# Performance work log

Hardware: AMD Instinct MI355X
Metric: run time of the kernel (lower is better)

Reference implementation:

```python
import jax, jax.numpy as jnp
import numpy as np

N, D, K = 500000, 128, 16
TEMPERATURE = 0.5
NUM_ITER = 10
EPS = 1e-8


def _row_normalize(x, eps=0.0):
    return x / (jnp.linalg.norm(x, axis=1, keepdims=True) + eps)


def _compute(data, mu, num_iter):
    # data: [N, D] (already L2-normalized rows), mu: [K, D]
    for _ in range(num_iter):
        mu = _row_normalize(mu)                      # mu / ||mu||
        # pairwise cosine similarity: re-normalizes both operands
        dn = _row_normalize(data)
        mn = _row_normalize(mu)
        cos = dn @ mn.T                              # [N, K]
        r = jax.nn.softmax(-TEMPERATURE * cos, axis=1)  # [N, K]
        cluster_r = r.sum(axis=0)                    # [K]
        cluster_mean = r.T @ data                    # [K, D]
        mu = cluster_mean / cluster_r[:, None]       # diag(1/cluster_r) @ mean
    return mu, r


def setup_inputs() -> dict:
    key = jax.random.key(0)
    k1, k2 = jax.random.split(key)
    embeddings = jax.random.normal(k1, (N, D), dtype=jnp.float32)
    mu_init = jax.random.uniform(k2, (K, D), dtype=jnp.float32)
    return {"embeddings": embeddings, "mu_init": mu_init}


def reference(embeddings, mu_init):
    data = embeddings / (jnp.linalg.norm(embeddings, axis=1) + EPS)[:, None]
    mu_init, _ = _compute(data, mu_init, 1)   # one warm-up iteration
    mu, r = _compute(data, mu_init, NUM_ITER)
    return (mu, r)
```

## Files before the change

kernel.cpp:

```cpp
#include <hip/hip_runtime.h>
#include <math.h>


#define N_ROWS 500000
#define D 128
#define K 16
#define TEMP 0.5f
#define EPSV 1e-8f
#define TILE 64
#define BLK 256
#define RL 20
#define NITER 11
#define NTILES ((N_ROWS + TILE - 1) / TILE)
#define NB 512

typedef const __attribute__((address_space(1))) float4* gas_f4;
typedef __attribute__((address_space(3))) float4* las_f4;

__device__ __forceinline__ void gl_lds16(const float4* g, float4* l) {
    __builtin_amdgcn_global_load_lds((gas_f4)g, (las_f4)l, 16, 0, 0);
}

__global__ void k_init(const float* __restrict__ mu0,
                       float* __restrict__ mn,
                       float* __restrict__ accum) {
    __shared__ float m1[K * D];
    __shared__ float inv[K];
    const int t = threadIdx.x;
    for (int i = t; i < K * D + K; i += 256) accum[i] = 0.0f;
    if (t < K) {
        float ss = 0.0f;
        for (int d = 0; d < D; ++d) { float v = mu0[t * D + d]; ss += v * v; }
        inv[t] = 1.0f / sqrtf(ss);
    }
    __syncthreads();
    for (int i = t; i < K * D; i += 256) m1[i] = mu0[i] * inv[i / D];
    __syncthreads();
    if (t < K) {
        float ss = 0.0f;
        for (int d = 0; d < D; ++d) { float v = m1[t * D + d]; ss += v * v; }
        inv[t] = 1.0f / sqrtf(ss);
    }
    __syncthreads();
    for (int i = t; i < K * D; i += 256) mn[i] = m1[i] * inv[i / D];
}

__global__ __launch_bounds__(BLK) void k_main(const float* __restrict__ e,
                                              const float* __restrict__ mn,
                                              float* __restrict__ accum,
                                              float* __restrict__ r_out,
                                              int write_r) {
    __shared__ float4 elds[2][TILE * 32];
    __shared__ float  mn_lds[K * D];
    __shared__ float  rlds[TILE * RL];

    const int t  = threadIdx.x;
    const int wv = t >> 6;
    const int ln = t & 63;
    const int g  = t >> 2;
    const int q  = t & 3;
    const int d4 = t & 31;
    const int kg = t >> 5;

    const float4* __restrict__ e4 = (const float4*)e;

    int tile = blockIdx.x;
    {
        #pragma unroll
        for (int i = 0; i < 8; ++i) {
            const int sigma = wv * 512 + i * 64 + ln;
            const int sg = sigma >> 5, s = sigma & 31;
            int row = tile * TILE + sg; if (row > N_ROWS - 1) row = N_ROWS - 1;
            gl_lds16(e4 + row * 32 + (s ^ (sg & 31)), &elds[0][wv * 512 + i * 64]);
        }
        const float4* mg = (const float4*)mn;
        float4* ml = (float4*)mn_lds;
        ml[t] = mg[t]; ml[t + 256] = mg[t + 256];
    }
    asm volatile("s_waitcnt lgkmcnt(0)" ::: "memory");
    __builtin_amdgcn_sched_barrier(0);
    __builtin_amdgcn_s_barrier();
    __builtin_amdgcn_sched_barrier(0);

    const float4* __restrict__ ml4 = (const float4*)mn_lds;

    float acc[2][4] = {{0.f,0.f,0.f,0.f},{0.f,0.f,0.f,0.f}};
    float crq[4] = {0.f, 0.f, 0.f, 0.f};

    int buf = 0;
    for (; tile < NTILES; tile += NB, buf ^= 1) {
        const int base = tile * TILE;
        const int nt = tile + NB;
        const bool hasnext = nt < NTILES;
        if (hasnext) {
            #pragma unroll
            for (int i = 0; i < 8; ++i) {
                const int sigma = wv * 512 + i * 64 + ln;
                const int sg = sigma >> 5, s = sigma & 31;
                int row = nt * TILE + sg; if (row > N_ROWS - 1) row = N_ROWS - 1;
                gl_lds16(e4 + row * 32 + (s ^ (sg & 31)), &elds[buf ^ 1][wv * 512 + i * 64]);
            }
            asm volatile("s_waitcnt vmcnt(8)" ::: "memory");
        } else {
            asm volatile("s_waitcnt vmcnt(0)" ::: "memory");
        }
        __builtin_amdgcn_sched_barrier(0);
        __builtin_amdgcn_s_barrier();
        __builtin_amdgcn_sched_barrier(0);

        const float4* __restrict__ eb = (const float4*)elds[buf];
        const int row = base + g;
        const bool valid = row < N_ROWS;

        float dot[K];
        #pragma unroll
        for (int k = 0; k < K; ++k) dot[k] = 0.0f;
        float ss = 0.0f;
        #pragma unroll
        for (int c = 0; c < 8; ++c) {
            const float4 ev = eb[(g << 5) + ((c * 4 + q) ^ (g & 31))];
            ss += ev.x * ev.x + ev.y * ev.y + ev.z * ev.z + ev.w * ev.w;
            #pragma unroll
            for (int k = 0; k < K; ++k) {
                const float4 m = ml4[k * 32 + c * 4 + q];
                dot[k] += ev.x * m.x + ev.y * m.y + ev.z * m.z + ev.w * m.w;
            }
        }
        #pragma unroll
        for (int k = 0; k < K; ++k) {
            dot[k] += __shfl_xor(dot[k], 1);
            dot[k] += __shfl_xor(dot[k], 2);
        }
        ss += __shfl_xor(ss, 1);
        ss += __shfl_xor(ss, 2);

        const float nrm  = sqrtf(ss);
        const float binv = 1.0f / nrm;
        const float ainv = 1.0f / (nrm + EPSV);

        float mx = -1e30f;
        #pragma unroll
        for (int k = 0; k < K; ++k) {
            dot[k] = -TEMP * dot[k] * binv;
            mx = fmaxf(mx, dot[k]);
        }
        float sum = 0.0f;
        #pragma unroll
        for (int k = 0; k < K; ++k) { dot[k] = __expf(dot[k] - mx); sum += dot[k]; }
        const float isum = 1.0f / sum;

        float rsel[4] = {0.f, 0.f, 0.f, 0.f};
        #pragma unroll
        for (int qq = 0; qq < 4; ++qq) {
            if (q == qq) {
                #pragma unroll
                for (int j = 0; j < 4; ++j) rsel[j] = dot[qq * 4 + j];
            }
        }
        float4 rv;
        rv.x = valid ? rsel[0] * isum : 0.0f;
        rv.y = valid ? rsel[1] * isum : 0.0f;
        rv.z = valid ? rsel[2] * isum : 0.0f;
        rv.w = valid ? rsel[3] * isum : 0.0f;
        crq[0] += rv.x; crq[1] += rv.y; crq[2] += rv.z; crq[3] += rv.w;

        float4 rt;
        rt.x = rv.x * ainv; rt.y = rv.y * ainv;
        rt.z = rv.z * ainv; rt.w = rv.w * ainv;
        *(float4*)&rlds[g * RL + q * 4] = rt;

        if (write_r && valid)
            ((float4*)(r_out + row * K))[q] = rv;

        asm volatile("s_waitcnt lgkmcnt(0)" ::: "memory");
        __builtin_amdgcn_sched_barrier(0);
        __builtin_amdgcn_s_barrier();
        __builtin_amdgcn_sched_barrier(0);

        #pragma unroll 8
        for (int p = 0; p < TILE; ++p) {
            const float4 ev = eb[(p << 5) + (d4 ^ (p & 31))];
            const float2 rr = *(const float2*)&rlds[p * RL + 2 * kg];
            acc[0][0] += rr.x * ev.x; acc[0][1] += rr.x * ev.y;
            acc[0][2] += rr.x * ev.z; acc[0][3] += rr.x * ev.w;
            acc[1][0] += rr.y * ev.x; acc[1][1] += rr.y * ev.y;
            acc[1][2] += rr.y * ev.z; acc[1][3] += rr.y * ev.w;
        }
        __builtin_amdgcn_sched_barrier(0);
        __builtin_amdgcn_s_barrier();
        __builtin_amdgcn_sched_barrier(0);
    }

    #pragma unroll
    for (int kk = 0; kk < 2; ++kk)
        #pragma unroll
        for (int j = 0; j < 4; ++j)
            atomicAdd(&accum[(2 * kg + kk) * D + d4 * 4 + j], acc[kk][j]);

    __syncthreads();
    *(float4*)&rlds[t * 4] = *(float4*)crq;
    __syncthreads();
    if (t < K) {
        const int qq = t >> 2, jj = t & 3;
        float s = 0.0f;
        #pragma unroll 4
        for (int i = 0; i < 64; ++i) s += rlds[(i * 4 + qq) * 4 + jj];
        atomicAdd(&accum[K * D + t], s);
    }
}

__global__ void k_update(float* __restrict__ accum,
                         float* __restrict__ mn,
                         float* __restrict__ mu_out,
                         int last) {
    __shared__ float mu[K * D];
    __shared__ float inv[K];
    const int t = threadIdx.x;
    for (int i = t; i < K * D; i += 256)
        mu[i] = accum[i] / accum[K * D + i / D];
    __syncthreads();
    if (last) {
        for (int i = t; i < K * D; i += 256) mu_out[i] = mu[i];
    } else {
        if (t < K) {
            float ssq = 0.0f;
            for (int d = 0; d < D; ++d) { float v = mu[t * D + d]; ssq += v * v; }
            inv[t] = 1.0f / sqrtf(ssq);
        }
        __syncthreads();
        for (int i = t; i < K * D; i += 256) mu[i] *= inv[i / D];
        __syncthreads();
        if (t < K) {
            float ssq = 0.0f;
            for (int d = 0; d < D; ++d) { float v = mu[t * D + d]; ssq += v * v; }
            inv[t] = 1.0f / sqrtf(ssq);
        }
        __syncthreads();
        for (int i = t; i < K * D; i += 256) mn[i] = mu[i] * inv[i / D];
    }
    __syncthreads();
    for (int i = t; i < K * D + K; i += 256) accum[i] = 0.0f;
}

extern "C" void kernel_launch(void* const* d_in, const int* in_sizes, int n_in,
                              void* d_out, int out_size, void* d_ws, size_t ws_size,
                              hipStream_t stream) {
    const float* e   = (const float*)d_in[0];
    const float* mu0 = (const float*)d_in[1];
    float* out = (float*)d_out;
    float* ws  = (float*)d_ws;

    float* mn    = ws;
    float* accum = ws + K * D;
    float* r_out = out + K * D;

    hipLaunchKernelGGL(k_init, dim3(1), dim3(256), 0, stream, mu0, mn, accum);
    for (int it = 0; it < NITER; ++it) {
        const int last = (it == NITER - 1) ? 1 : 0;
        hipLaunchKernelGGL(k_main, dim3(NB), dim3(BLK), 0, stream,
                           e, mn, accum, r_out, last);
        hipLaunchKernelGGL(k_update, dim3(1), dim3(256), 0, stream,
                           accum, mn, out, last);
    }
}
```

Before: 2.087 ms.

## Split dot products across waves by D-slice and read centroids from scalar memory

```diff
diff --git a/kernel.cpp b/kernel.cpp
--- a/kernel.cpp
+++ b/kernel.cpp
@@ -9,7 +9,6 @@
 #define EPSV 1e-8f
 #define TILE 64
 #define BLK 256
-#define RL 20
 #define NITER 11
 #define NTILES ((N_ROWS + TILE - 1) / TILE)
 #define NB 512
@@ -51,54 +50,46 @@
                                               float* __restrict__ r_out,
                                               int write_r) {
     __shared__ float4 elds[2][TILE * 32];
-    __shared__ float  mn_lds[K * D];
-    __shared__ float  rlds[TILE * RL];
-
-    const int t  = threadIdx.x;
-    const int wv = t >> 6;
-    const int ln = t & 63;
-    const int g  = t >> 2;
-    const int q  = t & 3;
-    const int d4 = t & 31;
-    const int kg = t >> 5;
-
-    const float4* __restrict__ e4 = (const float4*)e;
+    __shared__ float4 plds[4 * TILE * 4];
+
+    const int t   = threadIdx.x;
+    const int wvu = __builtin_amdgcn_readfirstlane(t >> 6);
+    const int ln  = t & 63;
+    const int g   = t >> 2;
+    const int q   = t & 3;
+    const int ph  = (t >> 5) & 1;
+    const int d4b = t & 31;
+
+    const float4* __restrict__ e4  = (const float4*)e;
+    const float4* __restrict__ mn4 = (const float4*)mn;
 
     int tile = blockIdx.x;
-    {
-        #pragma unroll
-        for (int i = 0; i < 8; ++i) {
-            const int sigma = wv * 512 + i * 64 + ln;
-            const int sg = sigma >> 5, s = sigma & 31;
-            int row = tile * TILE + sg; if (row > N_ROWS - 1) row = N_ROWS - 1;
-            gl_lds16(e4 + row * 32 + (s ^ (sg & 31)), &elds[0][wv * 512 + i * 64]);
-        }
-        const float4* mg = (const float4*)mn;
-        float4* ml = (float4*)mn_lds;
-        ml[t] = mg[t]; ml[t + 256] = mg[t + 256];
-    }
-    asm volatile("s_waitcnt lgkmcnt(0)" ::: "memory");
-    __builtin_amdgcn_sched_barrier(0);
-    __builtin_amdgcn_s_barrier();
-    __builtin_amdgcn_sched_barrier(0);
-
-    const float4* __restrict__ ml4 = (const float4*)mn_lds;
-
-    float acc[2][4] = {{0.f,0.f,0.f,0.f},{0.f,0.f,0.f,0.f}};
+    #pragma unroll
+    for (int i = 0; i < 8; ++i) {
+        const int sigma = wvu * 512 + i * 64 + ln;
+        const int sg = sigma >> 5, s = sigma & 31;
+        int row = tile * TILE + sg; if (row > N_ROWS - 1) row = N_ROWS - 1;
+        gl_lds16(e4 + row * 32 + (s ^ (sg & 31)), &elds[0][wvu * 512 + i * 64]);
+    }
+
+    float acc[4][4];
+    #pragma unroll
+    for (int a = 0; a < 4; ++a)
+        #pragma unroll
+        for (int b = 0; b < 4; ++b) acc[a][b] = 0.0f;
     float crq[4] = {0.f, 0.f, 0.f, 0.f};
 
     int buf = 0;
     for (; tile < NTILES; tile += NB, buf ^= 1) {
         const int base = tile * TILE;
         const int nt = tile + NB;
-        const bool hasnext = nt < NTILES;
-        if (hasnext) {
+        if (nt < NTILES) {
             #pragma unroll
             for (int i = 0; i < 8; ++i) {
-                const int sigma = wv * 512 + i * 64 + ln;
+                const int sigma = wvu * 512 + i * 64 + ln;
                 const int sg = sigma >> 5, s = sigma & 31;
                 int row = nt * TILE + sg; if (row > N_ROWS - 1) row = N_ROWS - 1;
-                gl_lds16(e4 + row * 32 + (s ^ (sg & 31)), &elds[buf ^ 1][wv * 512 + i * 64]);
+                gl_lds16(e4 + row * 32 + (s ^ (sg & 31)), &elds[buf ^ 1][wvu * 512 + i * 64]);
             }
             asm volatile("s_waitcnt vmcnt(8)" ::: "memory");
         } else {
@@ -109,82 +100,96 @@
         __builtin_amdgcn_sched_barrier(0);
 
         const float4* __restrict__ eb = (const float4*)elds[buf];
+
+        float dp[K];
+        #pragma unroll
+        for (int k = 0; k < K; ++k) dp[k] = 0.0f;
+        #pragma unroll
+        for (int c = 0; c < 8; ++c) {
+            const float4 ev = eb[(ln << 5) + (((c << 2) + wvu) ^ (ln & 31))];
+            #pragma unroll
+            for (int k = 0; k < K; ++k) {
+                const float4 m = mn4[k * 32 + (c << 2) + wvu];
+                dp[k] += ev.x * m.x + ev.y * m.y + ev.z * m.z + ev.w * m.w;
+            }
+        }
+        #pragma unroll
+        for (int j = 0; j < 4; ++j) {
+            float4 v;
+            v.x = dp[j * 4 + 0]; v.y = dp[j * 4 + 1];
+            v.z = dp[j * 4 + 2]; v.w = dp[j * 4 + 3];
+            plds[wvu * 256 + ln * 4 + ((j + (ln >> 1)) & 3)] = v;
+        }
+        asm volatile("s_waitcnt lgkmcnt(0)" ::: "memory");
+        __builtin_amdgcn_sched_barrier(0);
+        __builtin_amdgcn_s_barrier();
+        __builtin_amdgcn_sched_barrier(0);
+
         const int row = base + g;
         const bool valid = row < N_ROWS;
-
-        float dot[K];
-        #pragma unroll
-        for (int k = 0; k < K; ++k) dot[k] = 0.0f;
-        float ss = 0.0f;
+        float4 dsum = {0.f, 0.f, 0.f, 0.f};
+        #pragma unroll
+        for (int w2 = 0; w2 < 4; ++w2) {
+            const float4 v = plds[w2 * 256 + g * 4 + ((q + (g >> 1)) & 3)];
+            dsum.x += v.x; dsum.y += v.y; dsum.z += v.z; dsum.w += v.w;
+        }
+        float ssp = 0.0f;
         #pragma unroll
         for (int c = 0; c < 8; ++c) {
-            const float4 ev = eb[(g << 5) + ((c * 4 + q) ^ (g & 31))];
-            ss += ev.x * ev.x + ev.y * ev.y + ev.z * ev.z + ev.w * ev.w;
-            #pragma unroll
-            for (int k = 0; k < K; ++k) {
-                const float4 m = ml4[k * 32 + c * 4 + q];
-                dot[k] += ev.x * m.x + ev.y * m.y + ev.z * m.z + ev.w * m.w;
-            }
-        }
-        #pragma unroll
-        for (int k = 0; k < K; ++k) {
-            dot[k] += __shfl_xor(dot[k], 1);
-            dot[k] += __shfl_xor(dot[k], 2);
-        }
-        ss += __shfl_xor(ss, 1);
-        ss += __shfl_xor(ss, 2);
-
-        const float nrm  = sqrtf(ss);
+            const float4 evv = eb[(g << 5) + (((q << 3) + c) ^ (g & 31))];
+            ssp += evv.x * evv.x + evv.y * evv.y + evv.z * evv.z + evv.w * evv.w;
+        }
+        ssp += __shfl_xor(ssp, 1);
+        ssp += __shfl_xor(ssp, 2);
+        const float nrm  = sqrtf(ssp);
         const float binv = 1.0f / nrm;
         const float ainv = 1.0f / (nrm + EPSV);
 
-        float mx = -1e30f;
-        #pragma unroll
-        for (int k = 0; k < K; ++k) {
-            dot[k] = -TEMP * dot[k] * binv;
-            mx = fmaxf(mx, dot[k]);
-        }
-        float sum = 0.0f;
-        #pragma unroll
-        for (int k = 0; k < K; ++k) { dot[k] = __expf(dot[k] - mx); sum += dot[k]; }
-        const float isum = 1.0f / sum;
-
-        float rsel[4] = {0.f, 0.f, 0.f, 0.f};
-        #pragma unroll
-        for (int qq = 0; qq < 4; ++qq) {
-            if (q == qq) {
-                #pragma unroll
-                for (int j = 0; j < 4; ++j) rsel[j] = dot[qq * 4 + j];
-            }
-        }
-        float4 rv;
-        rv.x = valid ? rsel[0] * isum : 0.0f;
-        rv.y = valid ? rsel[1] * isum : 0.0f;
-        rv.z = valid ? rsel[2] * isum : 0.0f;
-        rv.w = valid ? rsel[3] * isum : 0.0f;
-        crq[0] += rv.x; crq[1] += rv.y; crq[2] += rv.z; crq[3] += rv.w;
+        float d0 = -TEMP * binv * dsum.x;
+        float d1 = -TEMP * binv * dsum.y;
+        float d2 = -TEMP * binv * dsum.z;
+        float d3 = -TEMP * binv * dsum.w;
+        float mx = fmaxf(fmaxf(d0, d1), fmaxf(d2, d3));
+        mx = fmaxf(mx, __shfl_xor(mx, 1));
+        mx = fmaxf(mx, __shfl_xor(mx, 2));
+        float e0 = __expf(d0 - mx), e1 = __expf(d1 - mx);
+        float e2 = __expf(d2 - mx), e3 = __expf(d3 - mx);
+        float sm = e0 + e1 + e2 + e3;
+        sm += __shfl_xor(sm, 1);
+        sm += __shfl_xor(sm, 2);
+        const float isum = 1.0f / sm;
+        const float r0 = valid ? e0 * isum : 0.0f;
+        const float r1 = valid ? e1 * isum : 0.0f;
+        const float r2 = valid ? e2 * isum : 0.0f;
+        const float r3 = valid ? e3 * isum : 0.0f;
+        crq[0] += r0; crq[1] += r1; crq[2] += r2; crq[3] += r3;
 
         float4 rt;
-        rt.x = rv.x * ainv; rt.y = rv.y * ainv;
-        rt.z = rv.z * ainv; rt.w = rv.w * ainv;
-        *(float4*)&rlds[g * RL + q * 4] = rt;
-
-        if (write_r && valid)
+        rt.x = r0 * ainv; rt.y = r1 * ainv; rt.z = r2 * ainv; rt.w = r3 * ainv;
+        plds[g * 4 + ((q + (g >> 1)) & 3)] = rt;
+
+        if (write_r && valid) {
+            float4 rv; rv.x = r0; rv.y = r1; rv.z = r2; rv.w = r3;
             ((float4*)(r_out + row * K))[q] = rv;
-
+        }
         asm volatile("s_waitcnt lgkmcnt(0)" ::: "memory");
         __builtin_amdgcn_sched_barrier(0);
         __builtin_amdgcn_s_barrier();
         __builtin_amdgcn_sched_barrier(0);
 
         #pragma unroll 8
-        for (int p = 0; p < TILE; ++p) {
-            const float4 ev = eb[(p << 5) + (d4 ^ (p & 31))];
-            const float2 rr = *(const float2*)&rlds[p * RL + 2 * kg];
+        for (int i = 0; i < 32; ++i) {
+            const int p = ph * 32 + i;
+            const float4 ev = eb[(p << 5) + (d4b ^ i)];
+            const float4 rr = plds[p * 4 + ((wvu + (p >> 1)) & 3)];
             acc[0][0] += rr.x * ev.x; acc[0][1] += rr.x * ev.y;
             acc[0][2] += rr.x * ev.z; acc[0][3] += rr.x * ev.w;
             acc[1][0] += rr.y * ev.x; acc[1][1] += rr.y * ev.y;
             acc[1][2] += rr.y * ev.z; acc[1][3] += rr.y * ev.w;
+            acc[2][0] += rr.z * ev.x; acc[2][1] += rr.z * ev.y;
+            acc[2][2] += rr.z * ev.z; acc[2][3] += rr.z * ev.w;
+            acc[3][0] += rr.w * ev.x; acc[3][1] += rr.w * ev.y;
+            acc[3][2] += rr.w * ev.z; acc[3][3] += rr.w * ev.w;
         }
         __builtin_amdgcn_sched_barrier(0);
         __builtin_amdgcn_s_barrier();
@@ -192,19 +197,21 @@
     }
 
     #pragma unroll
-    for (int kk = 0; kk < 2; ++kk)
+    for (int kk = 0; kk < 4; ++kk)
         #pragma unroll
         for (int j = 0; j < 4; ++j)
-            atomicAdd(&accum[(2 * kg + kk) * D + d4 * 4 + j], acc[kk][j]);
-
-    __syncthreads();
-    *(float4*)&rlds[t * 4] = *(float4*)crq;
+            atomicAdd(&accum[(wvu * 4 + kk) * D + d4b * 4 + j], acc[kk][j]);
+
+    __syncthreads();
+    float* fld = (float*)plds;
+    fld[t * 4 + 0] = crq[0]; fld[t * 4 + 1] = crq[1];
+    fld[t * 4 + 2] = crq[2]; fld[t * 4 + 3] = crq[3];
     __syncthreads();
     if (t < K) {
         const int qq = t >> 2, jj = t & 3;
         float s = 0.0f;
         #pragma unroll 4
-        for (int i = 0; i < 64; ++i) s += rlds[(i * 4 + qq) * 4 + jj];
+        for (int i = 0; i < 64; ++i) s += fld[(i * 4 + qq) * 4 + jj];
         atomicAdd(&accum[K * D + t], s);
     }
 }
```

Result: slower. 2.546 ms (+22.0%).

## Double block size to 512 threads and split work across 8 lanes per row

Applied to the files above, without the earlier changes.

```diff
diff --git a/kernel.cpp b/kernel.cpp
--- a/kernel.cpp
+++ b/kernel.cpp
@@ -8,8 +8,8 @@
 #define TEMP 0.5f
 #define EPSV 1e-8f
 #define TILE 64
-#define BLK 256
-#define RL 20
+#define BLK 512
+#define RL 18
 #define NITER 11
 #define NTILES ((N_ROWS + TILE - 1) / TILE)
 #define NB 512
@@ -51,56 +51,51 @@
                                               float* __restrict__ r_out,
                                               int write_r) {
     __shared__ float4 elds[2][TILE * 32];
-    __shared__ float  mn_lds[K * D];
+    __shared__ float4 mn_lds4[K * 32];
     __shared__ float  rlds[TILE * RL];
 
     const int t  = threadIdx.x;
     const int wv = t >> 6;
     const int ln = t & 63;
-    const int g  = t >> 2;
-    const int q  = t & 3;
+    const int g  = t >> 3;
+    const int o  = t & 7;
     const int d4 = t & 31;
-    const int kg = t >> 5;
+    const int kp = (t >> 5) & 7;
+    const int ph = t >> 8;
 
     const float4* __restrict__ e4 = (const float4*)e;
 
     int tile = blockIdx.x;
-    {
-        #pragma unroll
-        for (int i = 0; i < 8; ++i) {
-            const int sigma = wv * 512 + i * 64 + ln;
-            const int sg = sigma >> 5, s = sigma & 31;
-            int row = tile * TILE + sg; if (row > N_ROWS - 1) row = N_ROWS - 1;
-            gl_lds16(e4 + row * 32 + (s ^ (sg & 31)), &elds[0][wv * 512 + i * 64]);
-        }
-        const float4* mg = (const float4*)mn;
-        float4* ml = (float4*)mn_lds;
-        ml[t] = mg[t]; ml[t + 256] = mg[t + 256];
-    }
+    #pragma unroll
+    for (int i = 0; i < 4; ++i) {
+        const int sigma = wv * 256 + i * 64 + ln;
+        const int sg = sigma >> 5, s = sigma & 31;
+        int row = tile * TILE + sg; if (row > N_ROWS - 1) row = N_ROWS - 1;
+        gl_lds16(e4 + row * 32 + (s ^ (sg & 31)), &elds[0][sigma]);
+    }
+    mn_lds4[t] = ((const float4*)mn)[t & 511];
     asm volatile("s_waitcnt lgkmcnt(0)" ::: "memory");
     __builtin_amdgcn_sched_barrier(0);
     __builtin_amdgcn_s_barrier();
     __builtin_amdgcn_sched_barrier(0);
 
-    const float4* __restrict__ ml4 = (const float4*)mn_lds;
-
-    float acc[2][4] = {{0.f,0.f,0.f,0.f},{0.f,0.f,0.f,0.f}};
-    float crq[4] = {0.f, 0.f, 0.f, 0.f};
+    float acc0[4] = {0.f,0.f,0.f,0.f};
+    float acc1[4] = {0.f,0.f,0.f,0.f};
+    float cr0 = 0.f, cr1 = 0.f;
 
     int buf = 0;
     for (; tile < NTILES; tile += NB, buf ^= 1) {
         const int base = tile * TILE;
         const int nt = tile + NB;
-        const bool hasnext = nt < NTILES;
-        if (hasnext) {
+        if (nt < NTILES) {
             #pragma unroll
-            for (int i = 0; i < 8; ++i) {
-                const int sigma = wv * 512 + i * 64 + ln;
+            for (int i = 0; i < 4; ++i) {
+                const int sigma = wv * 256 + i * 64 + ln;
                 const int sg = sigma >> 5, s = sigma & 31;
                 int row = nt * TILE + sg; if (row > N_ROWS - 1) row = N_ROWS - 1;
-                gl_lds16(e4 + row * 32 + (s ^ (sg & 31)), &elds[buf ^ 1][wv * 512 + i * 64]);
+                gl_lds16(e4 + row * 32 + (s ^ (sg & 31)), &elds[buf ^ 1][sigma]);
             }
-            asm volatile("s_waitcnt vmcnt(8)" ::: "memory");
+            asm volatile("s_waitcnt vmcnt(4)" ::: "memory");
         } else {
             asm volatile("s_waitcnt vmcnt(0)" ::: "memory");
         }
@@ -112,65 +107,70 @@
         const int row = base + g;
         const bool valid = row < N_ROWS;
 
-        float dot[K];
-        #pragma unroll
-        for (int k = 0; k < K; ++k) dot[k] = 0.0f;
+        float dp[16];
+        #pragma unroll
+        for (int k = 0; k < 16; ++k) dp[k] = 0.0f;
         float ss = 0.0f;
         #pragma unroll
-        for (int c = 0; c < 8; ++c) {
-            const float4 ev = eb[(g << 5) + ((c * 4 + q) ^ (g & 31))];
+        for (int c = 0; c < 4; ++c) {
+            const float4 ev = eb[(g << 5) + (((c << 3) + o) ^ (g & 31))];
             ss += ev.x * ev.x + ev.y * ev.y + ev.z * ev.z + ev.w * ev.w;
             #pragma unroll
-            for (int k = 0; k < K; ++k) {
-                const float4 m = ml4[k * 32 + c * 4 + q];
-                dot[k] += ev.x * m.x + ev.y * m.y + ev.z * m.z + ev.w * m.w;
+            for (int k = 0; k < 16; ++k) {
+                const float4 m = mn_lds4[k * 32 + (c << 3) + o];
+                dp[k] += ev.x * m.x + ev.y * m.y + ev.z * m.z + ev.w * m.w;
             }
         }
         #pragma unroll
-        for (int k = 0; k < K; ++k) {
-            dot[k] += __shfl_xor(dot[k], 1);
-            dot[k] += __shfl_xor(dot[k], 2);
+        for (int k = 0; k < 16; ++k) {
+            dp[k] += __shfl_xor(dp[k], 1);
+            dp[k] += __shfl_xor(dp[k], 2);
         }
         ss += __shfl_xor(ss, 1);
         ss += __shfl_xor(ss, 2);
+        ss += __shfl_xor(ss, 4);
+
+        float q0 = dp[0], q1 = dp[1], q2 = dp[2], q3 = dp[3];
+        #pragma unroll
+        for (int mm = 1; mm < 4; ++mm) {
+            if ((o & 3) == mm) {
+                q0 = dp[4 * mm];     q1 = dp[4 * mm + 1];
+                q2 = dp[4 * mm + 2]; q3 = dp[4 * mm + 3];
+            }
+        }
+        q0 += __shfl_xor(q0, 4);
+        q1 += __shfl_xor(q1, 4);
+        q2 += __shfl_xor(q2, 4);
+        q3 += __shfl_xor(q3, 4);
+        const int hi = o >> 2;
+        const float s0 = hi ? q2 : q0;
+        const float s1 = hi ? q3 : q1;
+        const int ko = 4 * (o & 3) + 2 * hi;
 
         const float nrm  = sqrtf(ss);
         const float binv = 1.0f / nrm;
         const float ainv = 1.0f / (nrm + EPSV);
 
-        float mx = -1e30f;
-        #pragma unroll
-        for (int k = 0; k < K; ++k) {
-            dot[k] = -TEMP * dot[k] * binv;
-            mx = fmaxf(mx, dot[k]);
-        }
-        float sum = 0.0f;
-        #pragma unroll
-        for (int k = 0; k < K; ++k) { dot[k] = __expf(dot[k] - mx); sum += dot[k]; }
-        const float isum = 1.0f / sum;
-
-        float rsel[4] = {0.f, 0.f, 0.f, 0.f};
-        #pragma unroll
-        for (int qq = 0; qq < 4; ++qq) {
-            if (q == qq) {
-                #pragma unroll
-                for (int j = 0; j < 4; ++j) rsel[j] = dot[qq * 4 + j];
-            }
-        }
-        float4 rv;
-        rv.x = valid ? rsel[0] * isum : 0.0f;
-        rv.y = valid ? rsel[1] * isum : 0.0f;
-        rv.z = valid ? rsel[2] * isum : 0.0f;
-        rv.w = valid ? rsel[3] * isum : 0.0f;
-        crq[0] += rv.x; crq[1] += rv.y; crq[2] += rv.z; crq[3] += rv.w;
-
-        float4 rt;
-        rt.x = rv.x * ainv; rt.y = rv.y * ainv;
-        rt.z = rv.z * ainv; rt.w = rv.w * ainv;
-        *(float4*)&rlds[g * RL + q * 4] = rt;
-
+        const float dd0 = -TEMP * binv * s0;
+        const float dd1 = -TEMP * binv * s1;
+        float mx = fmaxf(dd0, dd1);
+        mx = fmaxf(mx, __shfl_xor(mx, 1));
+        mx = fmaxf(mx, __shfl_xor(mx, 2));
+        mx = fmaxf(mx, __shfl_xor(mx, 4));
+        const float e0 = __expf(dd0 - mx);
+        const float e1 = __expf(dd1 - mx);
+        float sm = e0 + e1;
+        sm += __shfl_xor(sm, 1);
+        sm += __shfl_xor(sm, 2);
+        sm += __shfl_xor(sm, 4);
+        const float isum = 1.0f / sm;
+        const float r0 = valid ? e0 * isum : 0.0f;
+        const float r1 = valid ? e1 * isum : 0.0f;
+        cr0 += r0; cr1 += r1;
+
+        *(float2*)&rlds[g * RL + ko] = make_float2(r0 * ainv, r1 * ainv);
         if (write_r && valid)
-            ((float4*)(r_out + row * K))[q] = rv;
+            *(float2*)(r_out + row * K + ko) = make_float2(r0, r1);
 
         asm volatile("s_waitcnt lgkmcnt(0)" ::: "memory");
         __builtin_amdgcn_sched_barrier(0);
@@ -178,13 +178,14 @@
         __builtin_amdgcn_sched_barrier(0);
 
         #pragma unroll 8
-        for (int p = 0; p < TILE; ++p) {
-            const float4 ev = eb[(p << 5) + (d4 ^ (p & 31))];
-            const float2 rr = *(const float2*)&rlds[p * RL + 2 * kg];
-            acc[0][0] += rr.x * ev.x; acc[0][1] += rr.x * ev.y;
-            acc[0][2] += rr.x * ev.z; acc[0][3] += rr.x * ev.w;
-            acc[1][0] += rr.y * ev.x; acc[1][1] += rr.y * ev.y;
-            acc[1][2] += rr.y * ev.z; acc[1][3] += rr.y * ev.w;
+        for (int i = 0; i < 32; ++i) {
+            const int p = (ph << 5) + i;
+            const float4 ev = eb[(p << 5) + (d4 ^ i)];
+            const float2 rr = *(const float2*)&rlds[p * RL + (kp << 1)];
+            acc0[0] += rr.x * ev.x; acc0[1] += rr.x * ev.y;
+            acc0[2] += rr.x * ev.z; acc0[3] += rr.x * ev.w;
+            acc1[0] += rr.y * ev.x; acc1[1] += rr.y * ev.y;
+            acc1[2] += rr.y * ev.z; acc1[3] += rr.y * ev.w;
         }
         __builtin_amdgcn_sched_barrier(0);
         __builtin_amdgcn_s_barrier();
@@ -192,19 +193,25 @@
     }
 
     #pragma unroll
-    for (int kk = 0; kk < 2; ++kk)
-        #pragma unroll
-        for (int j = 0; j < 4; ++j)
-            atomicAdd(&accum[(2 * kg + kk) * D + d4 * 4 + j], acc[kk][j]);
-
-    __syncthreads();
-    *(float4*)&rlds[t * 4] = *(float4*)crq;
+    for (int j = 0; j < 4; ++j)
+        atomicAdd(&accum[(2 * kp) * D + d4 * 4 + j], acc0[j]);
+    #pragma unroll
+    for (int j = 0; j < 4; ++j)
+        atomicAdd(&accum[(2 * kp + 1) * D + d4 * 4 + j], acc1[j]);
+
+    __syncthreads();
+    {
+        const int o2 = t & 7;
+        const int ko2 = 4 * (o2 & 3) + 2 * (o2 >> 2);
+        float* fld = (float*)rlds;
+        *(float2*)&fld[((t >> 3) << 4) + ko2] = make_float2(cr0, cr1);
+    }
     __syncthreads();
     if (t < K) {
-        const int qq = t >> 2, jj = t & 3;
+        float* fld = (float*)rlds;
         float s = 0.0f;
-        #pragma unroll 4
-        for (int i = 0; i < 64; ++i) s += rlds[(i * 4 + qq) * 4 + jj];
+        #pragma unroll 8
+        for (int gg = 0; gg < 64; ++gg) s += fld[gg * 16 + t];
         atomicAdd(&accum[K * D + t], s);
     }
 }
```

Result: slower. 2.907 ms (+39.3%).
